# Performance work log

Hardware: AMD Instinct MI355X
Metric: run time of the kernel (lower is better)

The kernel has to match this reference:

```python
import jax, jax.numpy as jnp
import numpy as np

B, S, D = 8, 1024, 1024
H, HD = 16, 64  # multiheads, head_dim; H*HD == D


def setup_inputs() -> dict:
    key = jax.random.key(0)
    ks = jax.random.split(key, 6)
    mk = lambda k, shape, scale=1.0: (jax.random.normal(k, shape, dtype=jnp.float32) * scale)
    return {
        "Q_seq": mk(ks[0], (B, S, D)),
        "K_seq": mk(ks[1], (B, S, D)),
        "V_seq": mk(ks[2], (B, S, D)),
        # nn.Linear weights stored as (out_features, in_features)
        "WQ": mk(ks[3], (H * HD, D), scale=D ** -0.5),
        "WK": mk(ks[4], (H * HD, D), scale=D ** -0.5),
        "WV": mk(ks[5], (H * HD, D), scale=D ** -0.5),
    }


def _attn(Q_seq, K_seq, V_seq, WQ, WK, WV):
    # projections (Linear: x @ W.T), then split heads -> [B, H, S, HD]
    def proj(x, W):
        y = jnp.einsum('bsd,od->bso', x, W)
        return y.reshape(x.shape[0], -1, H, HD).transpose(0, 2, 1, 3)
    Q, K, V = proj(Q_seq, WQ), proj(K_seq, WK), proj(V_seq, WV)
    scale = 1.0 / jnp.sqrt(jnp.float32(HD))
    scores = jnp.einsum('bhqd,bhkd->bhqk', Q, K) * scale  # [B,H,S,S]
    attn = jax.nn.softmax(scores, axis=-1)
    # dropout p=0.1 is identity in eval mode
    out = jnp.einsum('bhqk,bhkd->bhqd', attn, V)
    return out.transpose(0, 2, 1, 3).reshape(out.shape[0], -1, H * HD)


def reference(Q_seq, K_seq, V_seq, WQ, WK, WV):
    return _attn(Q_seq, K_seq, V_seq, WQ, WK, WV)
```

## Files before the change

kernel.cpp:

```cpp
#include <hip/hip_runtime.h>
#include <stdint.h>


#define B_N 8
#define S_N 1024
#define D_N 1024
#define H_N 16
#define HD_N 64
#define M_N (B_N * S_N)

typedef __bf16 bfrag __attribute__((ext_vector_type(8)));
typedef float f32x4 __attribute__((ext_vector_type(4)));
typedef float f32x16 __attribute__((ext_vector_type(16)));
typedef unsigned int u32;
typedef u32 u32x2 __attribute__((ext_vector_type(2)));
typedef u32 u32x4 __attribute__((ext_vector_type(4)));
typedef unsigned short u16;

__device__ __forceinline__ u16 f2bf(float f) {
  uint32_t u = __float_as_uint(f);
  u += 0x7FFFu + ((u >> 16) & 1u);
  return (u16)(u >> 16);
}

__device__ __forceinline__ void gl_lds16(const void* g, void* l) {
  __builtin_amdgcn_global_load_lds(
      (const __attribute__((address_space(1))) uint32_t*)g,
      (__attribute__((address_space(3))) uint32_t*)l, 16, 0, 0);
}

__device__ __forceinline__ u32 cvtpk(float lo, float hi) {
  u32 r;
  asm("v_cvt_pk_bf16_f32 %0, %1, %2" : "=v"(r) : "v"(lo), "v"(hi));
  return r;
}

__device__ __forceinline__ float exp2r(float x) {
#if __has_builtin(__builtin_amdgcn_exp2f)
  return __builtin_amdgcn_exp2f(x);
#else
  float r;
  asm("v_exp_f32 %0, %1" : "=v"(r) : "v"(x));
  return r;
#endif
}

__device__ __forceinline__ u32x2 pl32swap(u32 a, u32 b) {
#if __has_builtin(__builtin_amdgcn_permlane32_swap)
  return __builtin_amdgcn_permlane32_swap(a, b, false, false);
#else
  u32 sa = (u32)__shfl_xor((int)a, 32, 64), sb = (u32)__shfl_xor((int)b, 32, 64);
  const bool hi = (threadIdx.x & 32) != 0;
  u32x2 r;
  r[0] = hi ? sb : a;
  r[1] = hi ? b : sa;
  return r;
#endif
}

__device__ __forceinline__ float xhalf_max(float v) {
  u32x2 r = pl32swap(__float_as_uint(v), __float_as_uint(v));
  return fmaxf(__uint_as_float(r[0]), __uint_as_float(r[1]));
}
__device__ __forceinline__ float xhalf_add(float v) {
  u32x2 r = pl32swap(__float_as_uint(v), __float_as_uint(v));
  return __uint_as_float(r[0]) + __uint_as_float(r[1]);
}

__global__ __launch_bounds__(512, 1) void gemm_qkv(
    const float* __restrict__ Qs, const float* __restrict__ Ks,
    const float* __restrict__ Vs, const float* __restrict__ WQ,
    const float* __restrict__ WK, const float* __restrict__ WV,
    u16* __restrict__ Ybf) {
  const int bid = blockIdx.x;
  const int wid = (bid & 7) * 96 + (bid >> 3);
  const int mat = wid >> 8;
  const int rem = wid & 255;
  const int m0 = (rem >> 3) * 256;
  const int n0 = (rem & 7) * 128;

  const float* A = mat == 0 ? Qs : (mat == 1 ? Ks : Vs);
  const float* Bw = mat == 0 ? WQ : (mat == 1 ? WK : WV);
  u16* Y = Ybf + (size_t)mat * (M_N * D_N);

  __shared__ u16 Ast[2][4][4096];
  __shared__ u16 Bst[2][2][4096];

  const int t = threadIdx.x;
  const int w = t >> 6, l = t & 63;
  const int lr = l & 15, lg = l >> 4;
  const int wm = w >> 1, wn = w & 1;

  const float* aSrc = A + (size_t)(m0 + (t >> 3)) * D_N + (t & 7) * 8;
  const float* bSrc = Bw + (size_t)(n0 + (t >> 3)) * D_N + (t & 7) * 8;
  const int dst8 = (t >> 3) * 64 + ((((t & 7) ^ ((t >> 3) & 7))) << 3);

  const int asw = (lr & 7) << 3;
  const int koff0 = (lg * 8) ^ asw;
  const int koff1 = (32 + lg * 8) ^ asw;

  float4 ra[4][2], rw[2][2];

#define LOADT(tt)                                                             \
  do {                                                                        \
    _Pragma("unroll") for (int c_ = 0; c_ < 4; ++c_) {                        \
      ra[c_][0] = *(const float4*)(aSrc + (size_t)(c_ * 64) * D_N + (tt)*64); \
      ra[c_][1] =                                                             \
          *(const float4*)(aSrc + (size_t)(c_ * 64) * D_N + (tt)*64 + 4);     \
    }                                                                         \
    _Pragma("unroll") for (int c_ = 0; c_ < 2; ++c_) {                        \
      rw[c_][0] = *(const float4*)(bSrc + (size_t)(c_ * 64) * D_N + (tt)*64); \
      rw[c_][1] =                                                             \
          *(const float4*)(bSrc + (size_t)(c_ * 64) * D_N + (tt)*64 + 4);     \
    }                                                                         \
  } while (0)
#define WRITET(buf)                                                           \
  do {                                                                        \
    _Pragma("unroll") for (int c_ = 0; c_ < 4; ++c_) {                        \
      u32x4 pk_;                                                              \
      pk_[0] = cvtpk(ra[c_][0].x, ra[c_][0].y);                               \
      pk_[1] = cvtpk(ra[c_][0].z, ra[c_][0].w);                               \
      pk_[2] = cvtpk(ra[c_][1].x, ra[c_][1].y);                               \
      pk_[3] = cvtpk(ra[c_][1].z, ra[c_][1].w);                               \
      *(u32x4*)(&Ast[buf][c_][dst8]) = pk_;                                   \
    }                                                                         \
    _Pragma("unroll") for (int c_ = 0; c_ < 2; ++c_) {                        \
      u32x4 pk_;                                                              \
      pk_[0] = cvtpk(rw[c_][0].x, rw[c_][0].y);                               \
      pk_[1] = cvtpk(rw[c_][0].z, rw[c_][0].w);                               \
      pk_[2] = cvtpk(rw[c_][1].x, rw[c_][1].y);                               \
      pk_[3] = cvtpk(rw[c_][1].z, rw[c_][1].w);                               \
      *(u32x4*)(&Bst[buf][c_][dst8]) = pk_;                                   \
    }                                                                         \
  } while (0)
#define LDA8(AR, buf)                                                         \
  do {                                                                        \
    const u16* p_ = &Ast[buf][wm][lr * 64];                                   \
    _Pragma("unroll") for (int mf_ = 0; mf_ < 4; ++mf_) {                     \
      AR[mf_][0] = *(const bfrag*)(p_ + mf_ * 1024 + koff0);                  \
      AR[mf_][1] = *(const bfrag*)(p_ + mf_ * 1024 + koff1);                  \
    }                                                                         \
  } while (0)
#define LDB4(BR, buf, h)                                                      \
  do {                                                                        \
    const u16* p_ = &Bst[buf][wn][((h)*32 + lr) * 64];                        \
    BR[0][0] = *(const bfrag*)(p_ + koff0);                                   \
    BR[0][1] = *(const bfrag*)(p_ + koff1);                                   \
    BR[1][0] = *(const bfrag*)(p_ + 1024 + koff0);                            \
    BR[1][1] = *(const bfrag*)(p_ + 1024 + koff1);                            \
  } while (0)
#define MMAH(h, AR, BR)                                                       \
  do {                                                                        \
    __builtin_amdgcn_s_setprio(1);                                            \
    _Pragma("unroll") for (int mf_ = 0; mf_ < 4; ++mf_)                       \
    _Pragma("unroll") for (int j_ = 0; j_ < 2; ++j_)                          \
    _Pragma("unroll") for (int kk_ = 0; kk_ < 2; ++kk_)                       \
      acc[mf_][(h)*2 + j_] = __builtin_amdgcn_mfma_f32_16x16x32_bf16(         \
          AR[mf_][kk_], BR[j_][kk_], acc[mf_][(h)*2 + j_], 0, 0, 0);          \
    __builtin_amdgcn_s_setprio(0);                                            \
  } while (0)
#define BARR()                                                                \
  __builtin_amdgcn_s_barrier();                                               \
  __builtin_amdgcn_sched_barrier(0)
#define WAITL()                                                               \
  asm volatile("s_waitcnt lgkmcnt(0)" ::: "memory");                          \
  __builtin_amdgcn_sched_barrier(0)
#define WAITV0()                                                              \
  asm volatile("s_waitcnt vmcnt(0)" ::: "memory");                            \
  __builtin_amdgcn_sched_barrier(0)

  f32x4 acc[4][4];
#pragma unroll
  for (int i = 0; i < 4; ++i)
#pragma unroll
    for (int j = 0; j < 4; ++j) acc[i][j] = (f32x4){0.f, 0.f, 0.f, 0.f};

  LOADT(0);
  WAITV0();
  WRITET(0);
  LOADT(1);
  WAITL();
  BARR();

  for (int kt = 0; kt < 16; ++kt) {
    const int cb = kt & 1;
    bfrag a[4][2], b[2][2];
    LDA8(a, cb);
    LDB4(b, cb, 0);
    if (kt < 15) {
      WAITV0();
      WRITET(cb ^ 1);
      if (kt < 14) LOADT(kt + 2);
    }
    WAITL();
    MMAH(0, a, b);
    LDB4(b, cb, 1);
    WAITL();
    MMAH(1, a, b);
    BARR();
  }

  const float alpha = (mat == 0) ? 0.18033688011112042f : 1.0f;
  const int mrow = m0 + wm * 64;
  const int ncol = n0 + wn * 64;
  if (mat < 2) {
#pragma unroll
    for (int mf = 0; mf < 4; ++mf) {
      const int row0 = mrow + mf * 16 + lg * 4;
#pragma unroll
      for (int nf = 0; nf < 4; ++nf) {
        const int col = ncol + nf * 16 + lr;
#pragma unroll
        for (int r = 0; r < 4; ++r)
          Y[(size_t)(row0 + r) * D_N + col] = f2bf(acc[mf][nf][r] * alpha);
      }
    }
  } else {
    const int b = m0 >> 10;
#pragma unroll
    for (int mf = 0; mf < 4; ++mf) {
      const int s0 = (m0 & 1023) + wm * 64 + mf * 16 + lg * 4;
#pragma unroll
      for (int nf = 0; nf < 4; ++nf) {
        const int col = ncol + nf * 16 + lr;
        const f32x4 v = acc[mf][nf];
        ushort4 pk;
        pk.x = f2bf(v[0]); pk.y = f2bf(v[1]);
        pk.z = f2bf(v[2]); pk.w = f2bf(v[3]);
        *(ushort4*)(Y + (size_t)(b * D_N + col) * S_N + s0) = pk;
      }
    }
  }
#undef LOADT
#undef WRITET
#undef LDA8
#undef LDB4
#undef MMAH
#undef BARR
#undef WAITL
#undef WAITV0
}

union AttnSMem {
  struct { u16 K[3][4096]; u16 V[3][4096]; } st;
  float ol[4][32 * 34];
};

__global__ __launch_bounds__(256, 3) void attn_fwd(const u16* __restrict__ Yq,
                                                   const u16* __restrict__ Yk,
                                                   const u16* __restrict__ Yv,
                                                   float* __restrict__ out) {
  const int bid = blockIdx.x;
  const int wid = (bid & 7) * 128 + (bid >> 3);
  const int qt = wid & 7, bh = wid >> 3;
  const int b = bh >> 4, h = bh & 15;
  const int t = threadIdx.x, w = t >> 6, l = t & 63;
  const int ln = l & 31, hi = l >> 5;

  __shared__ AttnSMem sm;

  const int qbase = qt * 128 + w * 32;

  const int row0 = w * 8 + (l >> 3);
  const int srcoff = (((l & 7) ^ ((l >> 3) & 7)) << 3);
  const u16* kS0 = Yk + ((size_t)(b * S_N + row0) * D_N + h * HD_N + srcoff);
  const u16* vS0 = Yv + ((size_t)(b * D_N + h * HD_N + row0) * S_N + srcoff);

#define STAGE(buf, tt)                                                        \
  do {                                                                        \
    const u16* ka_ = kS0 + (size_t)(tt) * 64 * D_N;                           \
    const u16* va_ = vS0 + (tt) * 64;                                         \
    gl_lds16(ka_, sm.st.K[buf] + w * 512);                                    \
    gl_lds16(ka_ + (size_t)32 * D_N, sm.st.K[buf] + 2048 + w * 512);          \
    gl_lds16(va_, sm.st.V[buf] + w * 512);                                    \
    gl_lds16(va_ + (size_t)32 * S_N, sm.st.V[buf] + 2048 + w * 512);          \
  } while (0)

  bfrag qf[4];
  {
    const u16* qp = Yq + ((size_t)(b * S_N + qbase + ln) * D_N + h * HD_N + hi * 8);
#pragma unroll
    for (int c = 0; c < 4; ++c) qf[c] = *(const bfrag*)(qp + c * 16);
  }

  STAGE(0, 0);
  STAGE(1, 1);

  int kcol[4];
#pragma unroll
  for (int c = 0; c < 4; ++c)
    kcol[c] = (((c * 32 + hi * 16) ^ ((ln & 7) << 4)) >> 1);

  f32x16 o0, o1;
#pragma unroll
  for (int r = 0; r < 16; ++r) { o0[r] = 0.f; o1[r] = 0.f; }
  float m_r = -3.0e38f, l_r = 0.f;

  asm volatile("s_waitcnt vmcnt(4)" ::: "memory");
  __builtin_amdgcn_sched_barrier(0);
  __builtin_amdgcn_s_barrier();

  int rd = 0, sb = 2;
  for (int kt = 0; kt < 16; ++kt) {
    if (kt < 14) STAGE(sb, kt + 2);

    const u16* Kb = sm.st.K[rd];
    const u16* Vb = sm.st.V[rd];

    bfrag kf[8];
#pragma unroll
    for (int s2 = 0; s2 < 2; ++s2)
#pragma unroll
      for (int c = 0; c < 4; ++c)
        kf[s2 * 4 + c] = *(const bfrag*)(Kb + (s2 * 32 + ln) * 64 + kcol[c]);

    f32x16 sa, sbv;
#pragma unroll
    for (int r = 0; r < 16; ++r) { sa[r] = 0.f; sbv[r] = 0.f; }
    __builtin_amdgcn_s_setprio(1);
#pragma unroll
    for (int c = 0; c < 4; ++c) {
      sa = __builtin_amdgcn_mfma_f32_32x32x16_bf16(kf[c], qf[c], sa, 0, 0, 0);
      sbv = __builtin_amdgcn_mfma_f32_32x32x16_bf16(kf[4 + c], qf[c], sbv, 0, 0, 0);
    }
    __builtin_amdgcn_s_setprio(0);

    bfrag vf[8];
#pragma unroll
    for (int hf = 0; hf < 2; ++hf)
#pragma unroll
      for (int c = 0; c < 4; ++c)
        vf[hf * 4 + c] = *(const bfrag*)(Vb + (hf * 32 + ln) * 64 + kcol[c]);

    float t16[16];
#pragma unroll
    for (int r = 0; r < 16; ++r) t16[r] = fmaxf(sa[r], sbv[r]);
    float t8[8];
#pragma unroll
    for (int r = 0; r < 8; ++r) t8[r] = fmaxf(t16[r], t16[r + 8]);
    float t4[4];
#pragma unroll
    for (int r = 0; r < 4; ++r) t4[r] = fmaxf(t8[r], t8[r + 4]);
    float pmax = fmaxf(fmaxf(t4[0], t4[1]), fmaxf(t4[2], t4[3]));
    pmax = xhalf_max(pmax);

    if (__any(pmax > m_r + 8.f)) {
      const float mnew = fmaxf(m_r, pmax);
      const float corr = exp2r(m_r - mnew);
#pragma unroll
      for (int r = 0; r < 16; ++r) { o0[r] *= corr; o1[r] *= corr; }
      l_r *= corr;
      m_r = mnew;
    }

#pragma unroll
    for (int r = 0; r < 16; ++r) sa[r] = exp2r(sa[r] - m_r);
#pragma unroll
    for (int r = 0; r < 16; ++r) sbv[r] = exp2r(sbv[r] - m_r);
    float s16[16];
#pragma unroll
    for (int r = 0; r < 16; ++r) s16[r] = sa[r] + sbv[r];
    float s8[8];
#pragma unroll
    for (int r = 0; r < 8; ++r) s8[r] = s16[r] + s16[r + 8];
    float s4[4];
#pragma unroll
    for (int r = 0; r < 4; ++r) s4[r] = s8[r] + s8[r + 4];
    float rsum = (s4[0] + s4[1]) + (s4[2] + s4[3]);
    l_r += xhalf_add(rsum);

    __builtin_amdgcn_s_setprio(1);
#pragma unroll
    for (int c = 0; c < 4; ++c) {
      const int bs = (c & 1) * 8;
      float p0, p1, p2, p3, p4, p5, p6, p7;
      if (c < 2) {
        p0 = sa[bs + 0]; p1 = sa[bs + 1]; p2 = sa[bs + 2]; p3 = sa[bs + 3];
        p4 = sa[bs + 4]; p5 = sa[bs + 5]; p6 = sa[bs + 6]; p7 = sa[bs + 7];
      } else {
        p0 = sbv[bs + 0]; p1 = sbv[bs + 1]; p2 = sbv[bs + 2]; p3 = sbv[bs + 3];
        p4 = sbv[bs + 4]; p5 = sbv[bs + 5]; p6 = sbv[bs + 6]; p7 = sbv[bs + 7];
      }
      const u32 x1 = cvtpk(p0, p1), x2 = cvtpk(p2, p3);
      const u32 y1 = cvtpk(p4, p5), y2 = cvtpk(p6, p7);
      const u32x2 s1 = pl32swap(x1, y1);
      const u32x2 s2 = pl32swap(x2, y2);
      union { u32 u[4]; bfrag v; } pu;
      pu.u[0] = s1[0]; pu.u[1] = s2[0]; pu.u[2] = s1[1]; pu.u[3] = s2[1];
      o0 = __builtin_amdgcn_mfma_f32_32x32x16_bf16(vf[c], pu.v, o0, 0, 0, 0);
      o1 = __builtin_amdgcn_mfma_f32_32x32x16_bf16(vf[4 + c], pu.v, o1, 0, 0, 0);
    }
    __builtin_amdgcn_s_setprio(0);

    if (kt < 14) {
      asm volatile("s_waitcnt vmcnt(4)" ::: "memory");
    } else {
      asm volatile("s_waitcnt vmcnt(0)" ::: "memory");
    }
    __builtin_amdgcn_sched_barrier(0);
    __builtin_amdgcn_s_barrier();

    rd = (rd == 2) ? 0 : rd + 1;
    sb = (sb == 2) ? 0 : sb + 1;
  }

  const float inv = 1.f / l_r;
  float* ow = sm.ol[w];
  const int qr = l >> 1, ch = l & 1;
  const float* rp = ow + qr * 34 + ch * 16;
  float* op = out + ((size_t)(b * S_N + qbase + qr) * D_N + h * HD_N + ch * 16);

#pragma unroll
  for (int g = 0; g < 4; ++g) {
    f32x4 v;
#pragma unroll
    for (int j = 0; j < 4; ++j) v[j] = o0[g * 4 + j] * inv;
    *(f32x4*)(ow + ln * 34 + g * 8 + hi * 4) = v;
  }
  asm volatile("s_waitcnt lgkmcnt(0)" ::: "memory");
  __builtin_amdgcn_sched_barrier(0);
#pragma unroll
  for (int j = 0; j < 4; ++j)
    *(f32x4*)(op + j * 4) = *(const f32x4*)(rp + j * 4);
  asm volatile("s_waitcnt lgkmcnt(0)" ::: "memory");
  __builtin_amdgcn_sched_barrier(0);

#pragma unroll
  for (int g = 0; g < 4; ++g) {
    f32x4 v;
#pragma unroll
    for (int j = 0; j < 4; ++j) v[j] = o1[g * 4 + j] * inv;
    *(f32x4*)(ow + ln * 34 + g * 8 + hi * 4) = v;
  }
  asm volatile("s_waitcnt lgkmcnt(0)" ::: "memory");
  __builtin_amdgcn_sched_barrier(0);
#pragma unroll
  for (int j = 0; j < 4; ++j)
    *(f32x4*)(op + 32 + j * 4) = *(const f32x4*)(rp + j * 4);
#undef STAGE
}

extern "C" void kernel_launch(void* const* d_in, const int* in_sizes, int n_in,
                              void* d_out, int out_size, void* d_ws, size_t ws_size,
                              hipStream_t stream) {
  const float* Qs = (const float*)d_in[0];
  const float* Ks = (const float*)d_in[1];
  const float* Vs = (const float*)d_in[2];
  const float* WQ = (const float*)d_in[3];
  const float* WK = (const float*)d_in[4];
  const float* WV = (const float*)d_in[5];
  if (ws_size < 50331648ull) return;

  u16* Ybf = (u16*)d_ws;
  float* out = (float*)d_out;

  gemm_qkv<<<dim3(768), 512, 0, stream>>>(Qs, Ks, Vs, WQ, WK, WV, Ybf);
  attn_fwd<<<dim3(1024), 256, 0, stream>>>(Ybf, Ybf + 8388608, Ybf + 16777216, out);
}
```

Before: 142.7 us.

## Issue first MFMA half before LDS tile write and pack softmax reductions

In the projection GEMM loop, the first half of the MFMAs now runs before the global-to-LDS write and the next prefetch are issued, so matrix work overlaps the memory waits. In the attention softmax, the row max, the row sum and the output rescale now use two-wide float vectors, so the compiler can emit packed FP32 instructions (v_pk_add/v_pk_mul/v_pk_max style). The reordering changes when the vmcnt wait lands and may raise register pressure.

```diff
diff --git a/kernel.cpp b/kernel.cpp
--- a/kernel.cpp
+++ b/kernel.cpp
@@ -10,6 +10,7 @@
 #define M_N (B_N * S_N)
 
 typedef __bf16 bfrag __attribute__((ext_vector_type(8)));
+typedef float f32x2 __attribute__((ext_vector_type(2)));
 typedef float f32x4 __attribute__((ext_vector_type(4)));
 typedef float f32x16 __attribute__((ext_vector_type(16)));
 typedef unsigned int u32;
@@ -42,6 +43,17 @@
   float r;
   asm("v_exp_f32 %0, %1" : "=v"(r) : "v"(x));
   return r;
+#endif
+}
+
+__device__ __forceinline__ f32x2 mk2(float x, float y) {
+  f32x2 r; r[0] = x; r[1] = y; return r;
+}
+__device__ __forceinline__ f32x2 emax2(f32x2 a, f32x2 b) {
+#if __has_builtin(__builtin_elementwise_max)
+  return __builtin_elementwise_max(a, b);
+#else
+  return mk2(fmaxf(a[0], b[0]), fmaxf(a[1], b[1]));
 #endif
 }
 
@@ -187,13 +199,13 @@
     bfrag a[4][2], b[2][2];
     LDA8(a, cb);
     LDB4(b, cb, 0);
+    WAITL();
+    MMAH(0, a, b);
     if (kt < 15) {
       WAITV0();
       WRITET(cb ^ 1);
       if (kt < 14) LOADT(kt + 2);
     }
-    WAITL();
-    MMAH(0, a, b);
     LDB4(b, cb, 1);
     WAITL();
     MMAH(1, a, b);
@@ -332,23 +344,30 @@
       for (int c = 0; c < 4; ++c)
         vf[hf * 4 + c] = *(const bfrag*)(Vb + (hf * 32 + ln) * 64 + kcol[c]);
 
-    float t16[16];
-#pragma unroll
-    for (int r = 0; r < 16; ++r) t16[r] = fmaxf(sa[r], sbv[r]);
-    float t8[8];
-#pragma unroll
-    for (int r = 0; r < 8; ++r) t8[r] = fmaxf(t16[r], t16[r + 8]);
-    float t4[4];
-#pragma unroll
-    for (int r = 0; r < 4; ++r) t4[r] = fmaxf(t8[r], t8[r + 4]);
-    float pmax = fmaxf(fmaxf(t4[0], t4[1]), fmaxf(t4[2], t4[3]));
+    f32x2 t8[8];
+#pragma unroll
+    for (int r = 0; r < 8; ++r)
+      t8[r] = emax2(mk2(sa[2 * r], sa[2 * r + 1]),
+                    mk2(sbv[2 * r], sbv[2 * r + 1]));
+#pragma unroll
+    for (int r = 0; r < 4; ++r) t8[r] = emax2(t8[r], t8[r + 4]);
+    t8[0] = emax2(t8[0], t8[2]);
+    t8[1] = emax2(t8[1], t8[3]);
+    t8[0] = emax2(t8[0], t8[1]);
+    float pmax = fmaxf(t8[0][0], t8[0][1]);
     pmax = xhalf_max(pmax);
 
     if (__any(pmax > m_r + 8.f)) {
       const float mnew = fmaxf(m_r, pmax);
       const float corr = exp2r(m_r - mnew);
-#pragma unroll
-      for (int r = 0; r < 16; ++r) { o0[r] *= corr; o1[r] *= corr; }
+      const f32x2 cc = mk2(corr, corr);
+#pragma unroll
+      for (int r = 0; r < 8; ++r) {
+        f32x2 v0 = mk2(o0[2 * r], o0[2 * r + 1]) * cc;
+        f32x2 v1 = mk2(o1[2 * r], o1[2 * r + 1]) * cc;
+        o0[2 * r] = v0[0]; o0[2 * r + 1] = v0[1];
+        o1[2 * r] = v1[0]; o1[2 * r + 1] = v1[1];
+      }
       l_r *= corr;
       m_r = mnew;
     }
@@ -357,16 +376,16 @@
     for (int r = 0; r < 16; ++r) sa[r] = exp2r(sa[r] - m_r);
 #pragma unroll
     for (int r = 0; r < 16; ++r) sbv[r] = exp2r(sbv[r] - m_r);
-    float s16[16];
-#pragma unroll
-    for (int r = 0; r < 16; ++r) s16[r] = sa[r] + sbv[r];
-    float s8[8];
-#pragma unroll
-    for (int r = 0; r < 8; ++r) s8[r] = s16[r] + s16[r + 8];
-    float s4[4];
-#pragma unroll
-    for (int r = 0; r < 4; ++r) s4[r] = s8[r] + s8[r + 4];
-    float rsum = (s4[0] + s4[1]) + (s4[2] + s4[3]);
+    f32x2 s8v[8];
+#pragma unroll
+    for (int r = 0; r < 8; ++r)
+      s8v[r] = mk2(sa[2 * r], sa[2 * r + 1]) + mk2(sbv[2 * r], sbv[2 * r + 1]);
+#pragma unroll
+    for (int r = 0; r < 4; ++r) s8v[r] = s8v[r] + s8v[r + 4];
+    s8v[0] = s8v[0] + s8v[2];
+    s8v[1] = s8v[1] + s8v[3];
+    s8v[0] = s8v[0] + s8v[1];
+    float rsum = s8v[0][0] + s8v[0][1];
     l_r += xhalf_add(rsum);
 
     __builtin_amdgcn_s_setprio(1);
```

Measured after the change: 145.4 us. About the same (+1.9%).

## Shrink QKV GEMM tile to 128x128 with 256 threads, two blocks per CU

Applied to the files above, without the earlier changes.

The QKV projection GEMM moves from 512-thread blocks with 256x128 tiles to 256-thread blocks with 128x128 tiles. The grid doubles to 1536 blocks and the launch bounds allow two resident blocks per CU. The global-to-LDS staging is remapped so each thread loads 16 floats per row in four float4 chunks and writes two swizzled LDS vectors. The aim is better occupancy and latency hiding, at the cost of less A/B reuse per tile and more global traffic for the weights.

```diff
diff --git a/kernel.cpp b/kernel.cpp
--- a/kernel.cpp
+++ b/kernel.cpp
@@ -67,23 +67,23 @@
   return __uint_as_float(r[0]) + __uint_as_float(r[1]);
 }
 
-__global__ __launch_bounds__(512, 1) void gemm_qkv(
+__global__ __launch_bounds__(256, 2) void gemm_qkv(
     const float* __restrict__ Qs, const float* __restrict__ Ks,
     const float* __restrict__ Vs, const float* __restrict__ WQ,
     const float* __restrict__ WK, const float* __restrict__ WV,
     u16* __restrict__ Ybf) {
   const int bid = blockIdx.x;
-  const int wid = (bid & 7) * 96 + (bid >> 3);
-  const int mat = wid >> 8;
-  const int rem = wid & 255;
-  const int m0 = (rem >> 3) * 256;
+  const int wid = (bid & 7) * 192 + (bid >> 3);
+  const int mat = wid >> 9;
+  const int rem = wid & 511;
+  const int m0 = (rem >> 3) * 128;
   const int n0 = (rem & 7) * 128;
 
   const float* A = mat == 0 ? Qs : (mat == 1 ? Ks : Vs);
   const float* Bw = mat == 0 ? WQ : (mat == 1 ? WK : WV);
   u16* Y = Ybf + (size_t)mat * (M_N * D_N);
 
-  __shared__ u16 Ast[2][4][4096];
+  __shared__ u16 Ast[2][2][4096];
   __shared__ u16 Bst[2][2][4096];
 
   const int t = threadIdx.x;
@@ -91,46 +91,54 @@
   const int lr = l & 15, lg = l >> 4;
   const int wm = w >> 1, wn = w & 1;
 
-  const float* aSrc = A + (size_t)(m0 + (t >> 3)) * D_N + (t & 7) * 8;
-  const float* bSrc = Bw + (size_t)(n0 + (t >> 3)) * D_N + (t & 7) * 8;
-  const int dst8 = (t >> 3) * 64 + ((((t & 7) ^ ((t >> 3) & 7))) << 3);
+  const int srow = t >> 2, scol = (t & 3) * 16;
+  const float* aSrc = A + (size_t)(m0 + srow) * D_N + scol;
+  const float* bSrc = Bw + (size_t)(n0 + srow) * D_N + scol;
+  const int su = (t & 3) * 2;
+  const int dstw0 = srow * 64 + ((su ^ (srow & 7)) << 3);
+  const int dstw1 = srow * 64 + (((su + 1) ^ (srow & 7)) << 3);
 
   const int asw = (lr & 7) << 3;
   const int koff0 = (lg * 8) ^ asw;
   const int koff1 = (32 + lg * 8) ^ asw;
 
-  float4 ra[4][2], rw[2][2];
+  float4 ra[2][4], rw[2][4];
 
 #define LOADT(tt)                                                             \
   do {                                                                        \
-    _Pragma("unroll") for (int c_ = 0; c_ < 4; ++c_) {                        \
-      ra[c_][0] = *(const float4*)(aSrc + (size_t)(c_ * 64) * D_N + (tt)*64); \
-      ra[c_][1] =                                                             \
-          *(const float4*)(aSrc + (size_t)(c_ * 64) * D_N + (tt)*64 + 4);     \
+    _Pragma("unroll") for (int c_ = 0; c_ < 2; ++c_) {                        \
+      const float* pa_ = aSrc + (size_t)(c_ * 64) * D_N + (tt)*64;            \
+      const float* pb_ = bSrc + (size_t)(c_ * 64) * D_N + (tt)*64;            \
+      _Pragma("unroll") for (int j_ = 0; j_ < 4; ++j_) {                      \
+        ra[c_][j_] = *(const float4*)(pa_ + j_ * 4);                          \
+        rw[c_][j_] = *(const float4*)(pb_ + j_ * 4);                          \
+      }                                                                       \
     }                                                                         \
+  } while (0)
+#define WRITET(buf)                                                           \
+  do {                                                                        \
     _Pragma("unroll") for (int c_ = 0; c_ < 2; ++c_) {                        \
-      rw[c_][0] = *(const float4*)(bSrc + (size_t)(c_ * 64) * D_N + (tt)*64); \
-      rw[c_][1] =                                                             \
-          *(const float4*)(bSrc + (size_t)(c_ * 64) * D_N + (tt)*64 + 4);     \
-    }                                                                         \
-  } while (0)
-#define WRITET(buf)                                                           \
-  do {                                                                        \
-    _Pragma("unroll") for (int c_ = 0; c_ < 4; ++c_) {                        \
-      u32x4 pk_;                                                              \
-      pk_[0] = cvtpk(ra[c_][0].x, ra[c_][0].y);                               \
-      pk_[1] = cvtpk(ra[c_][0].z, ra[c_][0].w);                               \
-      pk_[2] = cvtpk(ra[c_][1].x, ra[c_][1].y);                               \
-      pk_[3] = cvtpk(ra[c_][1].z, ra[c_][1].w);                               \
-      *(u32x4*)(&Ast[buf][c_][dst8]) = pk_;                                   \
-    }                                                                         \
-    _Pragma("unroll") for (int c_ = 0; c_ < 2; ++c_) {                        \
-      u32x4 pk_;                                                              \
-      pk_[0] = cvtpk(rw[c_][0].x, rw[c_][0].y);                               \
-      pk_[1] = cvtpk(rw[c_][0].z, rw[c_][0].w);                               \
-      pk_[2] = cvtpk(rw[c_][1].x, rw[c_][1].y);                               \
-      pk_[3] = cvtpk(rw[c_][1].z, rw[c_][1].w);                               \
-      *(u32x4*)(&Bst[buf][c_][dst8]) = pk_;                                   \
+      u32x4 p0_, p1_;                                                         \
+      p0_[0] = cvtpk(ra[c_][0].x, ra[c_][0].y);                               \
+      p0_[1] = cvtpk(ra[c_][0].z, ra[c_][0].w);                               \
+      p0_[2] = cvtpk(ra[c_][1].x, ra[c_][1].y);                               \
+      p0_[3] = cvtpk(ra[c_][1].z, ra[c_][1].w);                               \
+      p1_[0] = cvtpk(ra[c_][2].x, ra[c_][2].y);                               \
+      p1_[1] = cvtpk(ra[c_][2].z, ra[c_][2].w);                               \
+      p1_[2] = cvtpk(ra[c_][3].x, ra[c_][3].y);                               \
+      p1_[3] = cvtpk(ra[c_][3].z, ra[c_][3].w);                               \
+      *(u32x4*)(&Ast[buf][c_][dstw0]) = p0_;                                  \
+      *(u32x4*)(&Ast[buf][c_][dstw1]) = p1_;                                  \
+      p0_[0] = cvtpk(rw[c_][0].x, rw[c_][0].y);                               \
+      p0_[1] = cvtpk(rw[c_][0].z, rw[c_][0].w);                               \
+      p0_[2] = cvtpk(rw[c_][1].x, rw[c_][1].y);                               \
+      p0_[3] = cvtpk(rw[c_][1].z, rw[c_][1].w);                               \
+      p1_[0] = cvtpk(rw[c_][2].x, rw[c_][2].y);                               \
+      p1_[1] = cvtpk(rw[c_][2].z, rw[c_][2].w);                               \
+      p1_[2] = cvtpk(rw[c_][3].x, rw[c_][3].y);                               \
+      p1_[3] = cvtpk(rw[c_][3].z, rw[c_][3].w);                               \
+      *(u32x4*)(&Bst[buf][c_][dstw0]) = p0_;                                  \
+      *(u32x4*)(&Bst[buf][c_][dstw1]) = p1_;                                  \
     }                                                                         \
   } while (0)
 #define LDA8(AR, buf)                                                         \
@@ -454,6 +462,6 @@
   u16* Ybf = (u16*)d_ws;
   float* out = (float*)d_out;
 
-  gemm_qkv<<<dim3(768), 512, 0, stream>>>(Qs, Ks, Vs, WQ, WK, WV, Ybf);
+  gemm_qkv<<<dim3(1536), 256, 0, stream>>>(Qs, Ks, Vs, WQ, WK, WV, Ybf);
   attn_fwd<<<dim3(1024), 256, 0, stream>>>(Ybf, Ybf + 8388608, Ybf + 16777216, out);
 }
```

Measured after the change: 169.3 us. +18.6%, slower.

## Software-pipeline QK^T of next tile with softmax/PV of current tile

Applied to the files above, without the earlier changes.

Restructures the attention loop so each iteration issues the QK^T MFMAs for tile kt+1 before running softmax and the PV MFMAs for tile kt. Two ping-pong score register sets carry scores between iterations. The K/V LDS ring grows from 3 to 4 stages, with loads prefetched three tiles ahead. The goal is to let matrix-core work overlap the exp/max/sum VALU work within a wave. In exchange it uses more registers and LDS per block, and the launch bounds drop from 3 to 2 blocks per CU, which lowers occupancy.

```diff
diff --git a/kernel.cpp b/kernel.cpp
--- a/kernel.cpp
+++ b/kernel.cpp
@@ -242,11 +242,11 @@
 }
 
 union AttnSMem {
-  struct { u16 K[3][4096]; u16 V[3][4096]; } st;
+  struct { u16 K[4][4096]; u16 V[4][4096]; } st;
   float ol[4][32 * 34];
 };
 
-__global__ __launch_bounds__(256, 3) void attn_fwd(const u16* __restrict__ Yq,
+__global__ __launch_bounds__(256, 2) void attn_fwd(const u16* __restrict__ Yq,
                                                    const u16* __restrict__ Yk,
                                                    const u16* __restrict__ Yv,
                                                    float* __restrict__ out) {
@@ -285,6 +285,7 @@
 
   STAGE(0, 0);
   STAGE(1, 1);
+  STAGE(2, 2);
 
   int kcol[4];
 #pragma unroll
@@ -300,108 +301,114 @@
   __builtin_amdgcn_sched_barrier(0);
   __builtin_amdgcn_s_barrier();
 
-  int rd = 0, sb = 2;
-  for (int kt = 0; kt < 16; ++kt) {
-    if (kt < 14) STAGE(sb, kt + 2);
-
-    const u16* Kb = sm.st.K[rd];
-    const u16* Vb = sm.st.V[rd];
-
-    bfrag kf[8];
-#pragma unroll
-    for (int s2 = 0; s2 < 2; ++s2)
-#pragma unroll
-      for (int c = 0; c < 4; ++c)
-        kf[s2 * 4 + c] = *(const bfrag*)(Kb + (s2 * 32 + ln) * 64 + kcol[c]);
-
-    f32x16 sa, sbv;
-#pragma unroll
-    for (int r = 0; r < 16; ++r) { sa[r] = 0.f; sbv[r] = 0.f; }
-    __builtin_amdgcn_s_setprio(1);
-#pragma unroll
-    for (int c = 0; c < 4; ++c) {
-      sa = __builtin_amdgcn_mfma_f32_32x32x16_bf16(kf[c], qf[c], sa, 0, 0, 0);
-      sbv = __builtin_amdgcn_mfma_f32_32x32x16_bf16(kf[4 + c], qf[c], sbv, 0, 0, 0);
-    }
-    __builtin_amdgcn_s_setprio(0);
-
-    bfrag vf[8];
-#pragma unroll
-    for (int hf = 0; hf < 2; ++hf)
-#pragma unroll
-      for (int c = 0; c < 4; ++c)
-        vf[hf * 4 + c] = *(const bfrag*)(Vb + (hf * 32 + ln) * 64 + kcol[c]);
-
-    float t16[16];
-#pragma unroll
-    for (int r = 0; r < 16; ++r) t16[r] = fmaxf(sa[r], sbv[r]);
-    float t8[8];
-#pragma unroll
-    for (int r = 0; r < 8; ++r) t8[r] = fmaxf(t16[r], t16[r + 8]);
-    float t4[4];
-#pragma unroll
-    for (int r = 0; r < 4; ++r) t4[r] = fmaxf(t8[r], t8[r + 4]);
-    float pmax = fmaxf(fmaxf(t4[0], t4[1]), fmaxf(t4[2], t4[3]));
-    pmax = xhalf_max(pmax);
-
-    if (__any(pmax > m_r + 8.f)) {
-      const float mnew = fmaxf(m_r, pmax);
-      const float corr = exp2r(m_r - mnew);
-#pragma unroll
-      for (int r = 0; r < 16; ++r) { o0[r] *= corr; o1[r] *= corr; }
-      l_r *= corr;
-      m_r = mnew;
-    }
-
-#pragma unroll
-    for (int r = 0; r < 16; ++r) sa[r] = exp2r(sa[r] - m_r);
-#pragma unroll
-    for (int r = 0; r < 16; ++r) sbv[r] = exp2r(sbv[r] - m_r);
-    float s16[16];
-#pragma unroll
-    for (int r = 0; r < 16; ++r) s16[r] = sa[r] + sbv[r];
-    float s8[8];
-#pragma unroll
-    for (int r = 0; r < 8; ++r) s8[r] = s16[r] + s16[r + 8];
-    float s4[4];
-#pragma unroll
-    for (int r = 0; r < 4; ++r) s4[r] = s8[r] + s8[r + 4];
-    float rsum = (s4[0] + s4[1]) + (s4[2] + s4[3]);
-    l_r += xhalf_add(rsum);
-
-    __builtin_amdgcn_s_setprio(1);
-#pragma unroll
-    for (int c = 0; c < 4; ++c) {
-      const int bs = (c & 1) * 8;
-      float p0, p1, p2, p3, p4, p5, p6, p7;
-      if (c < 2) {
-        p0 = sa[bs + 0]; p1 = sa[bs + 1]; p2 = sa[bs + 2]; p3 = sa[bs + 3];
-        p4 = sa[bs + 4]; p5 = sa[bs + 5]; p6 = sa[bs + 6]; p7 = sa[bs + 7];
-      } else {
-        p0 = sbv[bs + 0]; p1 = sbv[bs + 1]; p2 = sbv[bs + 2]; p3 = sbv[bs + 3];
-        p4 = sbv[bs + 4]; p5 = sbv[bs + 5]; p6 = sbv[bs + 6]; p7 = sbv[bs + 7];
-      }
-      const u32 x1 = cvtpk(p0, p1), x2 = cvtpk(p2, p3);
-      const u32 y1 = cvtpk(p4, p5), y2 = cvtpk(p6, p7);
-      const u32x2 s1 = pl32swap(x1, y1);
-      const u32x2 s2 = pl32swap(x2, y2);
-      union { u32 u[4]; bfrag v; } pu;
-      pu.u[0] = s1[0]; pu.u[1] = s2[0]; pu.u[2] = s1[1]; pu.u[3] = s2[1];
-      o0 = __builtin_amdgcn_mfma_f32_32x32x16_bf16(vf[c], pu.v, o0, 0, 0, 0);
-      o1 = __builtin_amdgcn_mfma_f32_32x32x16_bf16(vf[4 + c], pu.v, o1, 0, 0, 0);
-    }
-    __builtin_amdgcn_s_setprio(0);
-
-    if (kt < 14) {
-      asm volatile("s_waitcnt vmcnt(4)" ::: "memory");
-    } else {
-      asm volatile("s_waitcnt vmcnt(0)" ::: "memory");
-    }
-    __builtin_amdgcn_sched_barrier(0);
-    __builtin_amdgcn_s_barrier();
-
-    rd = (rd == 2) ? 0 : rd + 1;
-    sb = (sb == 2) ? 0 : sb + 1;
+#define QKT(BUFIDX, SA, SB)                                                   \
+  do {                                                                        \
+    const u16* Kb_ = sm.st.K[BUFIDX];                                         \
+    bfrag kf_[8];                                                             \
+    _Pragma("unroll") for (int s2_ = 0; s2_ < 2; ++s2_)                       \
+    _Pragma("unroll") for (int c_ = 0; c_ < 4; ++c_)                          \
+      kf_[s2_ * 4 + c_] =                                                     \
+          *(const bfrag*)(Kb_ + (s2_ * 32 + ln) * 64 + kcol[c_]);             \
+    _Pragma("unroll") for (int r_ = 0; r_ < 16; ++r_) {                       \
+      SA[r_] = 0.f; SB[r_] = 0.f;                                             \
+    }                                                                         \
+    __builtin_amdgcn_s_setprio(1);                                            \
+    _Pragma("unroll") for (int c_ = 0; c_ < 4; ++c_) {                        \
+      SA = __builtin_amdgcn_mfma_f32_32x32x16_bf16(kf_[c_], qf[c_], SA, 0, 0, 0); \
+      SB = __builtin_amdgcn_mfma_f32_32x32x16_bf16(kf_[4 + c_], qf[c_], SB, 0, 0, 0); \
+    }                                                                         \
+    __builtin_amdgcn_s_setprio(0);                                            \
+  } while (0)
+
+#define SMPV(SA, SB, VBUF)                                                    \
+  do {                                                                        \
+    const u16* Vb_ = sm.st.V[VBUF];                                           \
+    bfrag vf_[8];                                                             \
+    _Pragma("unroll") for (int hf_ = 0; hf_ < 2; ++hf_)                       \
+    _Pragma("unroll") for (int c_ = 0; c_ < 4; ++c_)                          \
+      vf_[hf_ * 4 + c_] =                                                     \
+          *(const bfrag*)(Vb_ + (hf_ * 32 + ln) * 64 + kcol[c_]);             \
+    float t16_[16];                                                           \
+    _Pragma("unroll") for (int r_ = 0; r_ < 16; ++r_)                         \
+        t16_[r_] = fmaxf(SA[r_], SB[r_]);                                     \
+    float t8_[8];                                                             \
+    _Pragma("unroll") for (int r_ = 0; r_ < 8; ++r_)                          \
+        t8_[r_] = fmaxf(t16_[r_], t16_[r_ + 8]);                              \
+    float t4_[4];                                                             \
+    _Pragma("unroll") for (int r_ = 0; r_ < 4; ++r_)                          \
+        t4_[r_] = fmaxf(t8_[r_], t8_[r_ + 4]);                                \
+    float pmax_ = fmaxf(fmaxf(t4_[0], t4_[1]), fmaxf(t4_[2], t4_[3]));        \
+    pmax_ = xhalf_max(pmax_);                                                 \
+    if (__any(pmax_ > m_r + 8.f)) {                                           \
+      const float mnew_ = fmaxf(m_r, pmax_);                                  \
+      const float corr_ = exp2r(m_r - mnew_);                                 \
+      _Pragma("unroll") for (int r_ = 0; r_ < 16; ++r_) {                     \
+        o0[r_] *= corr_; o1[r_] *= corr_;                                     \
+      }                                                                       \
+      l_r *= corr_;                                                           \
+      m_r = mnew_;                                                            \
+    }                                                                         \
+    _Pragma("unroll") for (int r_ = 0; r_ < 16; ++r_)                         \
+        SA[r_] = exp2r(SA[r_] - m_r);                                         \
+    _Pragma("unroll") for (int r_ = 0; r_ < 16; ++r_)                         \
+        SB[r_] = exp2r(SB[r_] - m_r);                                         \
+    float s16_[16];                                                           \
+    _Pragma("unroll") for (int r_ = 0; r_ < 16; ++r_)                         \
+        s16_[r_] = SA[r_] + SB[r_];                                           \
+    float s8_[8];                                                             \
+    _Pragma("unroll") for (int r_ = 0; r_ < 8; ++r_)                          \
+        s8_[r_] = s16_[r_] + s16_[r_ + 8];                                    \
+    float s4_[4];                                                             \
+    _Pragma("unroll") for (int r_ = 0; r_ < 4; ++r_)                          \
+        s4_[r_] = s8_[r_] + s8_[r_ + 4];                                      \
+    l_r += xhalf_add((s4_[0] + s4_[1]) + (s4_[2] + s4_[3]));                  \
+    __builtin_amdgcn_s_setprio(1);                                            \
+    _Pragma("unroll") for (int c_ = 0; c_ < 4; ++c_) {                        \
+      const int bs_ = (c_ & 1) * 8;                                           \
+      float p0_, p1_, p2_, p3_, p4_, p5_, p6_, p7_;                           \
+      if (c_ < 2) {                                                           \
+        p0_ = SA[bs_ + 0]; p1_ = SA[bs_ + 1]; p2_ = SA[bs_ + 2];              \
+        p3_ = SA[bs_ + 3]; p4_ = SA[bs_ + 4]; p5_ = SA[bs_ + 5];              \
+        p6_ = SA[bs_ + 6]; p7_ = SA[bs_ + 7];                                 \
+      } else {                                                                \
+        p0_ = SB[bs_ + 0]; p1_ = SB[bs_ + 1]; p2_ = SB[bs_ + 2];              \
+        p3_ = SB[bs_ + 3]; p4_ = SB[bs_ + 4]; p5_ = SB[bs_ + 5];              \
+        p6_ = SB[bs_ + 6]; p7_ = SB[bs_ + 7];                                 \
+      }                                                                       \
+      const u32 x1_ = cvtpk(p0_, p1_), x2_ = cvtpk(p2_, p3_);                 \
+      const u32 y1_ = cvtpk(p4_, p5_), y2_ = cvtpk(p6_, p7_);                 \
+      const u32x2 sw1_ = pl32swap(x1_, y1_);                                  \
+      const u32x2 sw2_ = pl32swap(x2_, y2_);                                  \
+      union { u32 u[4]; bfrag v; } pu_;                                       \
+      pu_.u[0] = sw1_[0]; pu_.u[1] = sw2_[0];                                 \
+      pu_.u[2] = sw1_[1]; pu_.u[3] = sw2_[1];                                 \
+      o0 = __builtin_amdgcn_mfma_f32_32x32x16_bf16(vf_[c_], pu_.v, o0, 0, 0, 0); \
+      o1 = __builtin_amdgcn_mfma_f32_32x32x16_bf16(vf_[4 + c_], pu_.v, o1, 0, 0, 0); \
+    }                                                                         \
+    __builtin_amdgcn_s_setprio(0);                                            \
+  } while (0)
+
+#define ITER(KT, INA, INB, OUTA, OUTB)                                        \
+  do {                                                                        \
+    if ((KT) < 13) STAGE(((KT) + 3) & 3, (KT) + 3);                           \
+    if ((KT) < 15) QKT(((KT) + 1) & 3, OUTA, OUTB);                           \
+    SMPV(INA, INB, (KT) & 3);                                                 \
+    if ((KT) < 13) {                                                          \
+      asm volatile("s_waitcnt vmcnt(4)" ::: "memory");                        \
+    } else {                                                                  \
+      asm volatile("s_waitcnt vmcnt(0)" ::: "memory");                        \
+    }                                                                         \
+    __builtin_amdgcn_sched_barrier(0);                                        \
+    __builtin_amdgcn_s_barrier();                                             \
+  } while (0)
+
+  f32x16 saE, sbE, saO, sbO;
+  QKT(0, saE, sbE);
+
+  for (int it = 0; it < 8; ++it) {
+    const int kt0 = 2 * it, kt1 = 2 * it + 1;
+    ITER(kt0, saE, sbE, saO, sbO);
+    ITER(kt1, saO, sbO, saE, sbE);
   }
 
   const float inv = 1.f / l_r;
@@ -438,6 +445,9 @@
   for (int j = 0; j < 4; ++j)
     *(f32x4*)(op + 32 + j * 4) = *(const f32x4*)(rp + j * 4);
 #undef STAGE
+#undef QKT
+#undef SMPV
+#undef ITER
 }
 
 extern "C" void kernel_launch(void* const* d_in, const int* in_sizes, int n_in,
```

New measurement: 142.8 us. About the same (+0.0%).
